# Optimization experiments

Hardware: AMD Instinct MI355X
Metric: run time of the kernel (lower is better)

Reference implementation:

```python
import jax, jax.numpy as jnp
import numpy as np


def _prelu(x, alpha):
    # PReLU with alpha shared over H,W (per-channel alpha, shape (C,))
    return jnp.where(x >= 0, x, alpha * x)


def _maxpool_2x2_s1_same(x):
    # TF MaxPooling2D(pool_size=2, strides=1, padding='same'): pad bottom/right
    return jax.lax.reduce_window(
        x, -jnp.inf, jax.lax.max,
        window_dimensions=(1, 2, 2, 1), window_strides=(1, 1, 1, 1),
        padding=[(0, 0), (0, 1), (0, 1), (0, 0)])


def _down_sample(x, W, b, alpha):
    # 1x1 Conv2D stride 2 'same' == subsample then channel matmul
    y = jnp.einsum('bhwc,cd->bhwd', x[:, ::2, ::2, :], W) + b
    y = _prelu(y, alpha)
    return _maxpool_2x2_s1_same(y)


def _up_sample(x, W, b, alpha):
    # 1x1 Conv2DTranspose stride 2 'same': even positions get conv output, rest only bias
    B, H, Wd, C = x.shape
    y = jnp.einsum('bhwc,cd->bhwd', x, W)
    z = jnp.zeros((B, 2 * H, 2 * Wd, C), dtype=x.dtype).at[:, ::2, ::2, :].set(y) + b
    z = _prelu(z, alpha)
    return _maxpool_2x2_s1_same(z)


def setup_inputs() -> dict:
    key = jax.random.key(0)
    ks = jax.random.split(key, 12)
    B, H, C = 8, 512, 3
    return {
        'input1': jax.random.normal(ks[0], (B, 2 * H, 2 * H, C), jnp.float32),
        'input2': jax.random.normal(ks[1], (B, H, H, C), jnp.float32),
        'input3': jax.random.normal(ks[2], (B, H // 2, H // 2, C), jnp.float32),
        'W_down': jax.random.normal(ks[3], (C, C), jnp.float32) * 0.5,
        'b_down': jax.random.normal(ks[4], (C,), jnp.float32) * 0.1,
        'alpha_down': jax.random.uniform(ks[5], (C,), jnp.float32) * 0.25,
        'W_up': jax.random.normal(ks[6], (C, C), jnp.float32) * 0.5,
        'b_up': jax.random.normal(ks[7], (C,), jnp.float32) * 0.1,
        'alpha_up': jax.random.uniform(ks[8], (C,), jnp.float32) * 0.25,
        'W_c': jax.random.normal(ks[9], (C, C), jnp.float32) * 0.5,
        'b_c': jax.random.normal(ks[10], (C,), jnp.float32) * 0.1,
        'alpha_g': jax.random.uniform(ks[11], (C,), jnp.float32) * 0.25,
        'scale': 2,
    }


def reference(input1, input2, input3, W_down, b_down, alpha_down,
              W_up, b_up, alpha_up, W_c, b_c, alpha_g, scale):
    assert scale == 2, 'only scale=2 path is well-defined in the source'
    i1 = _down_sample(input1, W_down, b_down, alpha_down)  # (B,H,W,C)
    i2 = input2
    i3 = _up_sample(input3, W_up, b_up, alpha_up)          # (B,H,W,C)

    s = i1 + i2 + i3
    g = jnp.mean(s, axis=(1, 2), keepdims=True)            # GlobalAvgPool, (B,1,1,C)

    conv1x1 = lambda t: jnp.einsum('bhwc,cd->bhwd', t, W_c) + b_c
    x = _prelu(conv1x1(g), alpha_g)
    # self.conv2d is the SAME layer applied three times -> c1 == c2 == c3,
    # hence y1 == y2 == y3; compute once (identical math).
    y = jax.nn.softmax(conv1x1(x), axis=-1)                # (B,1,1,C)
    return y * i1 + y * i2 + y * i3
```

## Files before the change

kernel.cpp:

```cpp
#include <hip/hip_runtime.h>

#define HW 512
#define NB 8

__device__ __forceinline__ float prelu(float x, float a) { return x >= 0.f ? x : a * x; }

__global__ __launch_bounds__(256) void k1_compute_s(
    const float* __restrict__ in1, const float* __restrict__ in2, const float* __restrict__ in3,
    const float* __restrict__ Wd, const float* __restrict__ bd, const float* __restrict__ ad,
    const float* __restrict__ Wu, const float* __restrict__ bu, const float* __restrict__ au,
    float* __restrict__ s_out, float* __restrict__ partials)
{
    const int b  = blockIdx.z;
    const int h0 = blockIdx.y * 16, w0 = blockIdx.x * 16;
    const int tid = threadIdx.x;

    __shared__ float d1[17][17][3];

    for (int idx = tid; idx < 17 * 17; idx += 256) {
        const int ty = idx / 17, tx = idx % 17;
        const int gh = h0 + ty, gw = w0 + tx;
        float v0 = -INFINITY, v1 = -INFINITY, v2 = -INFINITY;
        if (gh < HW && gw < HW) {
            const float* p = in1 + (((b * 1024 + 2 * gh) * 1024 + 2 * gw) * 3);
            const float x0 = p[0], x1 = p[1], x2 = p[2];
            v0 = prelu(x0 * Wd[0] + x1 * Wd[3] + x2 * Wd[6] + bd[0], ad[0]);
            v1 = prelu(x0 * Wd[1] + x1 * Wd[4] + x2 * Wd[7] + bd[1], ad[1]);
            v2 = prelu(x0 * Wd[2] + x1 * Wd[5] + x2 * Wd[8] + bd[2], ad[2]);
        }
        d1[ty][tx][0] = v0; d1[ty][tx][1] = v1; d1[ty][tx][2] = v2;
    }
    __syncthreads();

    const int ty = tid >> 4, tx = tid & 15;
    const int h = h0 + ty, w = w0 + tx;

    float i1c0 = fmaxf(fmaxf(d1[ty][tx][0], d1[ty][tx + 1][0]),
                       fmaxf(d1[ty + 1][tx][0], d1[ty + 1][tx + 1][0]));
    float i1c1 = fmaxf(fmaxf(d1[ty][tx][1], d1[ty][tx + 1][1]),
                       fmaxf(d1[ty + 1][tx][1], d1[ty + 1][tx + 1][1]));
    float i1c2 = fmaxf(fmaxf(d1[ty][tx][2], d1[ty][tx + 1][2]),
                       fmaxf(d1[ty + 1][tx][2], d1[ty + 1][tx + 1][2]));

    const float cu0 = prelu(bu[0], au[0]);
    const float cu1 = prelu(bu[1], au[1]);
    const float cu2 = prelu(bu[2], au[2]);
    float i3c0 = cu0, i3c1 = cu1, i3c2 = cu2;
    const int he = h + (h & 1), we = w + (w & 1);
    if (he < HW && we < HW) {
        const float* p = in3 + (((b * 256 + (he >> 1)) * 256 + (we >> 1)) * 3);
        const float x0 = p[0], x1 = p[1], x2 = p[2];
        i3c0 = fmaxf(i3c0, prelu(x0 * Wu[0] + x1 * Wu[3] + x2 * Wu[6] + bu[0], au[0]));
        i3c1 = fmaxf(i3c1, prelu(x0 * Wu[1] + x1 * Wu[4] + x2 * Wu[7] + bu[1], au[1]));
        i3c2 = fmaxf(i3c2, prelu(x0 * Wu[2] + x1 * Wu[5] + x2 * Wu[8] + bu[2], au[2]));
    }

    const int pix = ((b * HW + h) * HW + w) * 3;
    float s0 = i1c0 + in2[pix + 0] + i3c0;
    float s1 = i1c1 + in2[pix + 1] + i3c1;
    float s2 = i1c2 + in2[pix + 2] + i3c2;

    s_out[pix + 0] = s0; s_out[pix + 1] = s1; s_out[pix + 2] = s2;

    #pragma unroll
    for (int off = 32; off > 0; off >>= 1) {
        s0 += __shfl_down(s0, off);
        s1 += __shfl_down(s1, off);
        s2 += __shfl_down(s2, off);
    }
    __shared__ float red[4][3];
    const int lane = tid & 63, wave = tid >> 6;
    if (lane == 0) { red[wave][0] = s0; red[wave][1] = s1; red[wave][2] = s2; }
    __syncthreads();
    if (tid == 0) {
        const int pid = (b * 32 + blockIdx.y) * 32 + blockIdx.x;
        partials[pid * 3 + 0] = red[0][0] + red[1][0] + red[2][0] + red[3][0];
        partials[pid * 3 + 1] = red[0][1] + red[1][1] + red[2][1] + red[3][1];
        partials[pid * 3 + 2] = red[0][2] + red[1][2] + red[2][2] + red[3][2];
    }
}

__global__ __launch_bounds__(256) void k2_gate(
    const float* __restrict__ partials,
    const float* __restrict__ Wc, const float* __restrict__ bc, const float* __restrict__ ag,
    float* __restrict__ y)
{
    const int b = blockIdx.x;
    const int tid = threadIdx.x;
    float s0 = 0.f, s1 = 0.f, s2 = 0.f;
    for (int i = tid; i < 1024; i += 256) {
        const float* p = partials + (b * 1024 + i) * 3;
        s0 += p[0]; s1 += p[1]; s2 += p[2];
    }
    #pragma unroll
    for (int off = 32; off > 0; off >>= 1) {
        s0 += __shfl_down(s0, off);
        s1 += __shfl_down(s1, off);
        s2 += __shfl_down(s2, off);
    }
    __shared__ float red[4][3];
    const int lane = tid & 63, wave = tid >> 6;
    if (lane == 0) { red[wave][0] = s0; red[wave][1] = s1; red[wave][2] = s2; }
    __syncthreads();
    if (tid == 0) {
        const float inv_n = 1.f / (float)(HW * HW);
        const float g0 = (red[0][0] + red[1][0] + red[2][0] + red[3][0]) * inv_n;
        const float g1 = (red[0][1] + red[1][1] + red[2][1] + red[3][1]) * inv_n;
        const float g2 = (red[0][2] + red[1][2] + red[2][2] + red[3][2]) * inv_n;
        const float x0 = prelu(g0 * Wc[0] + g1 * Wc[3] + g2 * Wc[6] + bc[0], ag[0]);
        const float x1 = prelu(g0 * Wc[1] + g1 * Wc[4] + g2 * Wc[7] + bc[1], ag[1]);
        const float x2 = prelu(g0 * Wc[2] + g1 * Wc[5] + g2 * Wc[8] + bc[2], ag[2]);
        const float q0 = x0 * Wc[0] + x1 * Wc[3] + x2 * Wc[6] + bc[0];
        const float q1 = x0 * Wc[1] + x1 * Wc[4] + x2 * Wc[7] + bc[1];
        const float q2 = x0 * Wc[2] + x1 * Wc[5] + x2 * Wc[8] + bc[2];
        const float m = fmaxf(q0, fmaxf(q1, q2));
        const float e0 = expf(q0 - m), e1 = expf(q1 - m), e2 = expf(q2 - m);
        const float inv = 1.f / (e0 + e1 + e2);
        y[b * 3 + 0] = e0 * inv;
        y[b * 3 + 1] = e1 * inv;
        y[b * 3 + 2] = e2 * inv;
    }
}

__global__ __launch_bounds__(256) void k3_scale(float* __restrict__ out, const float* __restrict__ y)
{
    const int i = blockIdx.x * 256 + threadIdx.x;
    const int f = i * 4;
    const int b = f / (HW * HW * 3);
    const int c0 = f % 3;
    const float* yb = y + b * 3;
    const float m0 = yb[c0];
    const float m1 = yb[c0 == 2 ? 0 : c0 + 1];
    const float m2 = yb[c0 == 0 ? 2 : c0 - 1];
    float4 v = reinterpret_cast<float4*>(out)[i];
    v.x *= m0; v.y *= m1; v.z *= m2; v.w *= m0;
    reinterpret_cast<float4*>(out)[i] = v;
}

extern "C" void kernel_launch(void* const* d_in, const int* in_sizes, int n_in,
                              void* d_out, int out_size, void* d_ws, size_t ws_size,
                              hipStream_t stream)
{
    const float* in1 = (const float*)d_in[0];
    const float* in2 = (const float*)d_in[1];
    const float* in3 = (const float*)d_in[2];
    const float* Wd  = (const float*)d_in[3];
    const float* bd  = (const float*)d_in[4];
    const float* ad  = (const float*)d_in[5];
    const float* Wu  = (const float*)d_in[6];
    const float* bu  = (const float*)d_in[7];
    const float* au  = (const float*)d_in[8];
    const float* Wc  = (const float*)d_in[9];
    const float* bc  = (const float*)d_in[10];
    const float* ag  = (const float*)d_in[11];
    float* out = (float*)d_out;

    float* partials = (float*)d_ws;
    float* y        = partials + 8192 * 3;

    k1_compute_s<<<dim3(32, 32, NB), 256, 0, stream>>>(in1, in2, in3, Wd, bd, ad, Wu, bu, au, out, partials);
    k2_gate<<<NB, 256, 0, stream>>>(partials, Wc, bc, ag, y);
    k3_scale<<<6144, 256, 0, stream>>>(out, y);
}
```

Baseline: 39.07 us.

## Fuse all stages into one cooperative kernel holding the sum in LDS

Replaces the three-kernel pipeline with a single cooperative-launch kernel of 256 blocks of 1024 threads. Each block handles a 16-row stripe of one batch image, keeps the intermediate sum in shared memory, and performs a grid-wide sync before computing the gate and writing scaled output directly. This removes the global write and re-read of the intermediate sum plus two extra launches, at the cost of a grid barrier, about 117KB of LDS per block and one block per CU. The old kernels remain as a fallback if the cooperative launch fails.

New measurement: 84.42 us. +116.1%, slower.

```diff
diff --git a/kernel.cpp b/kernel.cpp
--- a/kernel.cpp
+++ b/kernel.cpp
@@ -1,9 +1,143 @@
 #include <hip/hip_runtime.h>
+#include <hip/hip_cooperative_groups.h>
+
+namespace cg = cooperative_groups;
 
 #define HW 512
-#define NB 8
 
 __device__ __forceinline__ float prelu(float x, float a) { return x >= 0.f ? x : a * x; }
+
+__global__ __launch_bounds__(1024) void fused(
+    const float* __restrict__ in1, const float* __restrict__ in2, const float* __restrict__ in3,
+    const float* __restrict__ Wd, const float* __restrict__ bd, const float* __restrict__ ad,
+    const float* __restrict__ Wu, const float* __restrict__ bu, const float* __restrict__ au,
+    const float* __restrict__ Wc, const float* __restrict__ bc, const float* __restrict__ ag,
+    float* __restrict__ out, float* __restrict__ ws)
+{
+    extern __shared__ float smem[];
+    float* s_lds = smem;
+    float* d1    = smem + 24576;
+    float* red   = d1 + 4617;
+    float* ybuf  = red + 48;
+
+    const int tid    = threadIdx.x;
+    const int bid    = blockIdx.x;
+    const int batch  = bid >> 5;
+    const int stripe = bid & 31;
+    const int r0     = stripe * 16;
+
+    float wd[9], wu[9];
+    #pragma unroll
+    for (int k = 0; k < 9; k++) { wd[k] = Wd[k]; wu[k] = Wu[k]; }
+    const float bd0 = bd[0], bd1 = bd[1], bd2 = bd[2];
+    const float ad0 = ad[0], ad1 = ad[1], ad2 = ad[2];
+    const float bu0 = bu[0], bu1 = bu[1], bu2 = bu[2];
+    const float au0 = au[0], au1 = au[1], au2 = au[2];
+    const float cu0 = prelu(bu0, au0), cu1 = prelu(bu1, au1), cu2 = prelu(bu2, au2);
+
+    float p0 = 0.f, p1 = 0.f, p2 = 0.f;
+    const int lrOff = tid >> 9;
+    const int col   = tid & 511;
+
+    for (int i = 0; i < 8; i++) {
+        const int drStart = (i == 0) ? 0 : (2 * i + 1);
+        const int n = (2 * i + 2 - drStart + 1) * 513;
+        __syncthreads();
+        for (int e = tid; e < n; e += 1024) {
+            const int dr = drStart + e / 513;
+            const int c  = e - (e / 513) * 513;
+            const int gh = r0 + dr;
+            float v0 = -INFINITY, v1 = -INFINITY, v2 = -INFINITY;
+            if (gh < HW && c < HW) {
+                const float* p = in1 + ((batch * 1024 + 2 * gh) * 1024 + 2 * c) * 3;
+                const float x0 = p[0], x1 = p[1], x2 = p[2];
+                v0 = prelu(x0 * wd[0] + x1 * wd[3] + x2 * wd[6] + bd0, ad0);
+                v1 = prelu(x0 * wd[1] + x1 * wd[4] + x2 * wd[7] + bd1, ad1);
+                v2 = prelu(x0 * wd[2] + x1 * wd[5] + x2 * wd[8] + bd2, ad2);
+            }
+            float* q = d1 + (dr % 3) * 1539 + c * 3;
+            q[0] = v0; q[1] = v1; q[2] = v2;
+        }
+        __syncthreads();
+
+        const int lr  = 2 * i + lrOff;
+        const int row = r0 + lr;
+        const float* ra = d1 + (lr % 3) * 1539 + col * 3;
+        const float* rb = d1 + ((lr + 1) % 3) * 1539 + col * 3;
+        float i1c0 = fmaxf(fmaxf(ra[0], ra[3]), fmaxf(rb[0], rb[3]));
+        float i1c1 = fmaxf(fmaxf(ra[1], ra[4]), fmaxf(rb[1], rb[4]));
+        float i1c2 = fmaxf(fmaxf(ra[2], ra[5]), fmaxf(rb[2], rb[5]));
+
+        float i3c0 = cu0, i3c1 = cu1, i3c2 = cu2;
+        const int he = row + (row & 1), we = col + (col & 1);
+        if (he < HW && we < HW) {
+            const float* p = in3 + ((batch * 256 + (he >> 1)) * 256 + (we >> 1)) * 3;
+            const float x0 = p[0], x1 = p[1], x2 = p[2];
+            i3c0 = fmaxf(i3c0, prelu(x0 * wu[0] + x1 * wu[3] + x2 * wu[6] + bu0, au0));
+            i3c1 = fmaxf(i3c1, prelu(x0 * wu[1] + x1 * wu[4] + x2 * wu[7] + bu1, au1));
+            i3c2 = fmaxf(i3c2, prelu(x0 * wu[2] + x1 * wu[5] + x2 * wu[8] + bu2, au2));
+        }
+
+        const float* q2 = in2 + ((batch * HW + row) * HW + col) * 3;
+        const float s0 = i1c0 + q2[0] + i3c0;
+        const float s1 = i1c1 + q2[1] + i3c1;
+        const float s2 = i1c2 + q2[2] + i3c2;
+        float* qs = s_lds + (lr * 512 + col) * 3;
+        qs[0] = s0; qs[1] = s1; qs[2] = s2;
+        p0 += s0; p1 += s1; p2 += s2;
+    }
+
+    #pragma unroll
+    for (int off = 32; off > 0; off >>= 1) {
+        p0 += __shfl_down(p0, off);
+        p1 += __shfl_down(p1, off);
+        p2 += __shfl_down(p2, off);
+    }
+    const int lane = tid & 63, wv = tid >> 6;
+    if (lane == 0) { red[wv * 3 + 0] = p0; red[wv * 3 + 1] = p1; red[wv * 3 + 2] = p2; }
+    __syncthreads();
+    if (tid == 0) {
+        float t0 = 0.f, t1 = 0.f, t2 = 0.f;
+        for (int k = 0; k < 16; k++) { t0 += red[k * 3]; t1 += red[k * 3 + 1]; t2 += red[k * 3 + 2]; }
+        ws[bid * 3 + 0] = t0; ws[bid * 3 + 1] = t1; ws[bid * 3 + 2] = t2;
+        __threadfence();
+    }
+
+    cg::this_grid().sync();
+
+    if (tid == 0) {
+        float g0 = 0.f, g1 = 0.f, g2 = 0.f;
+        const float* pw = ws + batch * 96;
+        for (int k = 0; k < 32; k++) { g0 += pw[k * 3]; g1 += pw[k * 3 + 1]; g2 += pw[k * 3 + 2]; }
+        const float inv_n = 1.f / (float)(HW * HW);
+        g0 *= inv_n; g1 *= inv_n; g2 *= inv_n;
+        const float x0 = prelu(g0 * Wc[0] + g1 * Wc[3] + g2 * Wc[6] + bc[0], ag[0]);
+        const float x1 = prelu(g0 * Wc[1] + g1 * Wc[4] + g2 * Wc[7] + bc[1], ag[1]);
+        const float x2 = prelu(g0 * Wc[2] + g1 * Wc[5] + g2 * Wc[8] + bc[2], ag[2]);
+        const float q0 = x0 * Wc[0] + x1 * Wc[3] + x2 * Wc[6] + bc[0];
+        const float q1 = x0 * Wc[1] + x1 * Wc[4] + x2 * Wc[7] + bc[1];
+        const float q2 = x0 * Wc[2] + x1 * Wc[5] + x2 * Wc[8] + bc[2];
+        const float m  = fmaxf(q0, fmaxf(q1, q2));
+        const float e0 = expf(q0 - m), e1 = expf(q1 - m), e2 = expf(q2 - m);
+        const float inv = 1.f / (e0 + e1 + e2);
+        ybuf[0] = e0 * inv; ybuf[1] = e1 * inv; ybuf[2] = e2 * inv;
+    }
+    __syncthreads();
+    const float ym[3] = { ybuf[0], ybuf[1], ybuf[2] };
+
+    float4* og = (float4*)(out + (size_t)bid * 24576);
+    #pragma unroll
+    for (int k = 0; k < 6; k++) {
+        const int idx = k * 1024 + tid;
+        const int c0  = idx % 3;
+        float4 v = *((const float4*)s_lds + idx);
+        v.x *= ym[c0];
+        v.y *= ym[c0 == 2 ? 0 : c0 + 1];
+        v.z *= ym[c0 == 0 ? 2 : c0 - 1];
+        v.w *= ym[c0];
+        og[idx] = v;
+    }
+}
 
 __global__ __launch_bounds__(256) void k1_compute_s(
     const float* __restrict__ in1, const float* __restrict__ in2, const float* __restrict__ in3,
@@ -14,9 +148,7 @@
     const int b  = blockIdx.z;
     const int h0 = blockIdx.y * 16, w0 = blockIdx.x * 16;
     const int tid = threadIdx.x;
-
     __shared__ float d1[17][17][3];
-
     for (int idx = tid; idx < 17 * 17; idx += 256) {
         const int ty = idx / 17, tx = idx % 17;
         const int gh = h0 + ty, gw = w0 + tx;
@@ -31,20 +163,12 @@
         d1[ty][tx][0] = v0; d1[ty][tx][1] = v1; d1[ty][tx][2] = v2;
     }
     __syncthreads();
-
     const int ty = tid >> 4, tx = tid & 15;
     const int h = h0 + ty, w = w0 + tx;
-
-    float i1c0 = fmaxf(fmaxf(d1[ty][tx][0], d1[ty][tx + 1][0]),
-                       fmaxf(d1[ty + 1][tx][0], d1[ty + 1][tx + 1][0]));
-    float i1c1 = fmaxf(fmaxf(d1[ty][tx][1], d1[ty][tx + 1][1]),
-                       fmaxf(d1[ty + 1][tx][1], d1[ty + 1][tx + 1][1]));
-    float i1c2 = fmaxf(fmaxf(d1[ty][tx][2], d1[ty][tx + 1][2]),
-                       fmaxf(d1[ty + 1][tx][2], d1[ty + 1][tx + 1][2]));
-
-    const float cu0 = prelu(bu[0], au[0]);
-    const float cu1 = prelu(bu[1], au[1]);
-    const float cu2 = prelu(bu[2], au[2]);
+    float i1c0 = fmaxf(fmaxf(d1[ty][tx][0], d1[ty][tx + 1][0]), fmaxf(d1[ty + 1][tx][0], d1[ty + 1][tx + 1][0]));
+    float i1c1 = fmaxf(fmaxf(d1[ty][tx][1], d1[ty][tx + 1][1]), fmaxf(d1[ty + 1][tx][1], d1[ty + 1][tx + 1][1]));
+    float i1c2 = fmaxf(fmaxf(d1[ty][tx][2], d1[ty][tx + 1][2]), fmaxf(d1[ty + 1][tx][2], d1[ty + 1][tx + 1][2]));
+    const float cu0 = prelu(bu[0], au[0]), cu1 = prelu(bu[1], au[1]), cu2 = prelu(bu[2], au[2]);
     float i3c0 = cu0, i3c1 = cu1, i3c2 = cu2;
     const int he = h + (h & 1), we = w + (w & 1);
     if (he < HW && we < HW) {
@@ -54,19 +178,14 @@
         i3c1 = fmaxf(i3c1, prelu(x0 * Wu[1] + x1 * Wu[4] + x2 * Wu[7] + bu[1], au[1]));
         i3c2 = fmaxf(i3c2, prelu(x0 * Wu[2] + x1 * Wu[5] + x2 * Wu[8] + bu[2], au[2]));
     }
-
     const int pix = ((b * HW + h) * HW + w) * 3;
     float s0 = i1c0 + in2[pix + 0] + i3c0;
     float s1 = i1c1 + in2[pix + 1] + i3c1;
     float s2 = i1c2 + in2[pix + 2] + i3c2;
-
     s_out[pix + 0] = s0; s_out[pix + 1] = s1; s_out[pix + 2] = s2;
-
     #pragma unroll
     for (int off = 32; off > 0; off >>= 1) {
-        s0 += __shfl_down(s0, off);
-        s1 += __shfl_down(s1, off);
-        s2 += __shfl_down(s2, off);
+        s0 += __shfl_down(s0, off); s1 += __shfl_down(s1, off); s2 += __shfl_down(s2, off);
     }
     __shared__ float red[4][3];
     const int lane = tid & 63, wave = tid >> 6;
@@ -94,9 +213,7 @@
     }
     #pragma unroll
     for (int off = 32; off > 0; off >>= 1) {
-        s0 += __shfl_down(s0, off);
-        s1 += __shfl_down(s1, off);
-        s2 += __shfl_down(s2, off);
+        s0 += __shfl_down(s0, off); s1 += __shfl_down(s1, off); s2 += __shfl_down(s2, off);
     }
     __shared__ float red[4][3];
     const int lane = tid & 63, wave = tid >> 6;
@@ -116,9 +233,7 @@
         const float m = fmaxf(q0, fmaxf(q1, q2));
         const float e0 = expf(q0 - m), e1 = expf(q1 - m), e2 = expf(q2 - m);
         const float inv = 1.f / (e0 + e1 + e2);
-        y[b * 3 + 0] = e0 * inv;
-        y[b * 3 + 1] = e1 * inv;
-        y[b * 3 + 2] = e2 * inv;
+        y[b * 3 + 0] = e0 * inv; y[b * 3 + 1] = e1 * inv; y[b * 3 + 2] = e2 * inv;
     }
 }
 
@@ -154,11 +269,21 @@
     const float* bc  = (const float*)d_in[10];
     const float* ag  = (const float*)d_in[11];
     float* out = (float*)d_out;
-
-    float* partials = (float*)d_ws;
-    float* y        = partials + 8192 * 3;
-
-    k1_compute_s<<<dim3(32, 32, NB), 256, 0, stream>>>(in1, in2, in3, Wd, bd, ad, Wu, bu, au, out, partials);
-    k2_gate<<<NB, 256, 0, stream>>>(partials, Wc, bc, ag, y);
-    k3_scale<<<6144, 256, 0, stream>>>(out, y);
-}
+    float* ws  = (float*)d_ws;
+
+    void* args[] = { (void*)&in1, (void*)&in2, (void*)&in3,
+                     (void*)&Wd, (void*)&bd, (void*)&ad,
+                     (void*)&Wu, (void*)&bu, (void*)&au,
+                     (void*)&Wc, (void*)&bc, (void*)&ag,
+                     (void*)&out, (void*)&ws };
+    const unsigned smem_bytes = (24576 + 4617 + 48 + 3 + 4) * sizeof(float);
+    hipError_t err = hipLaunchCooperativeKernel((const void*)fused, dim3(256), dim3(1024),
+                                                args, smem_bytes, stream);
+    if (err != hipSuccess) {
+        float* partials = ws;
+        float* y        = partials + 8192 * 3;
+        k1_compute_s<<<dim3(32, 32, 8), 256, 0, stream>>>(in1, in2, in3, Wd, bd, ad, Wu, bu, au, out, partials);
+        k2_gate<<<8, 256, 0, stream>>>(partials, Wc, bc, ag, y);
+        k3_scale<<<6144, 256, 0, stream>>>(out, y);
+    }
+}
```

## Widen k1 tiles to 4 pixels per thread and fuse gate into scale kernel

Applied to the files above, without the earlier changes.

The first kernel now has each thread handle 4 consecutive pixels in a 16x64 tile. Weights are held in registers, and the in2 reads and s writes use float4 vector accesses, so there are fewer partial sums. The gate computation is folded into the scaling kernel: every block recomputes the per-batch softmax from 256 partials. This removes one launch and the separate y buffer. The cost is redundant gate math in each of 1024 blocks, plus more register use and a higher LDS footprint per block.

Measured after the change: 42.67 us. 9.2% more time.

```diff
diff --git a/kernel.cpp b/kernel.cpp
--- a/kernel.cpp
+++ b/kernel.cpp
@@ -1,7 +1,7 @@
 #include <hip/hip_runtime.h>
 
 #define HW 512
-#define NB 8
+#define D1_PITCH 197
 
 __device__ __forceinline__ float prelu(float x, float a) { return x >= 0.f ? x : a * x; }
 
@@ -11,130 +11,175 @@
     const float* __restrict__ Wu, const float* __restrict__ bu, const float* __restrict__ au,
     float* __restrict__ s_out, float* __restrict__ partials)
 {
-    const int b  = blockIdx.z;
-    const int h0 = blockIdx.y * 16, w0 = blockIdx.x * 16;
-    const int tid = threadIdx.x;
-
-    __shared__ float d1[17][17][3];
-
-    for (int idx = tid; idx < 17 * 17; idx += 256) {
-        const int ty = idx / 17, tx = idx % 17;
-        const int gh = h0 + ty, gw = w0 + tx;
-        float v0 = -INFINITY, v1 = -INFINITY, v2 = -INFINITY;
-        if (gh < HW && gw < HW) {
-            const float* p = in1 + (((b * 1024 + 2 * gh) * 1024 + 2 * gw) * 3);
+    __shared__ float d1[17 * D1_PITCH];
+    __shared__ float red[4][3];
+
+    const int tid   = threadIdx.x;
+    const int bx    = blockIdx.x;
+    const int by    = blockIdx.y;
+    const int batch = blockIdx.z;
+    const int h0    = by * 16;
+    const int w0b   = bx * 64;
+
+    float wd[9], wu[9];
+    #pragma unroll
+    for (int k = 0; k < 9; k++) { wd[k] = Wd[k]; wu[k] = Wu[k]; }
+    const float bd0 = bd[0], bd1 = bd[1], bd2 = bd[2];
+    const float ad0 = ad[0], ad1 = ad[1], ad2 = ad[2];
+    const float bu0 = bu[0], bu1 = bu[1], bu2 = bu[2];
+    const float au0 = au[0], au1 = au[1], au2 = au[2];
+    const float cu0 = prelu(bu0, au0), cu1 = prelu(bu1, au1), cu2 = prelu(bu2, au2);
+
+    #pragma unroll
+    for (int k = 0; k < 5; ++k) {
+        const int e = k * 256 + tid;
+        if (e < 17 * 65) {
+            const int dr = e / 65, dc = e - dr * 65;
+            const int gh = h0 + dr, gw = w0b + dc;
+            float v0 = -INFINITY, v1 = -INFINITY, v2 = -INFINITY;
+            if (gh < HW && gw < HW) {
+                const float* p = in1 + ((size_t)((batch * 1024 + 2 * gh) * 1024 + 2 * gw)) * 3;
+                const float x0 = p[0], x1 = p[1], x2 = p[2];
+                v0 = prelu(x0 * wd[0] + x1 * wd[3] + x2 * wd[6] + bd0, ad0);
+                v1 = prelu(x0 * wd[1] + x1 * wd[4] + x2 * wd[7] + bd1, ad1);
+                v2 = prelu(x0 * wd[2] + x1 * wd[5] + x2 * wd[8] + bd2, ad2);
+            }
+            float* q = d1 + dr * D1_PITCH + dc * 3;
+            q[0] = v0; q[1] = v1; q[2] = v2;
+        }
+    }
+    __syncthreads();
+
+    const int r  = tid >> 4;
+    const int cg = tid & 15;
+    const int h  = h0 + r;
+    const int w0 = w0b + cg * 4;
+
+    const float* in2p = in2 + ((size_t)((batch * HW + h) * HW + w0)) * 3;
+    float i2v[12];
+    #pragma unroll
+    for (int k = 0; k < 3; ++k)
+        *reinterpret_cast<float4*>(&i2v[4 * k]) = reinterpret_cast<const float4*>(in2p)[k];
+
+    const int he = h + (h & 1);
+    const bool heok = he < HW;
+    const int w3 = w0 >> 1;
+    float ud[3][3];
+    #pragma unroll
+    for (int k = 0; k < 3; ++k) {
+        float u0 = cu0, u1 = cu1, u2 = cu2;
+        if (heok && (w3 + k) < 256) {
+            const float* p = in3 + ((size_t)((batch * 256 + (he >> 1)) * 256 + w3 + k)) * 3;
             const float x0 = p[0], x1 = p[1], x2 = p[2];
-            v0 = prelu(x0 * Wd[0] + x1 * Wd[3] + x2 * Wd[6] + bd[0], ad[0]);
-            v1 = prelu(x0 * Wd[1] + x1 * Wd[4] + x2 * Wd[7] + bd[1], ad[1]);
-            v2 = prelu(x0 * Wd[2] + x1 * Wd[5] + x2 * Wd[8] + bd[2], ad[2]);
-        }
-        d1[ty][tx][0] = v0; d1[ty][tx][1] = v1; d1[ty][tx][2] = v2;
-    }
-    __syncthreads();
-
-    const int ty = tid >> 4, tx = tid & 15;
-    const int h = h0 + ty, w = w0 + tx;
-
-    float i1c0 = fmaxf(fmaxf(d1[ty][tx][0], d1[ty][tx + 1][0]),
-                       fmaxf(d1[ty + 1][tx][0], d1[ty + 1][tx + 1][0]));
-    float i1c1 = fmaxf(fmaxf(d1[ty][tx][1], d1[ty][tx + 1][1]),
-                       fmaxf(d1[ty + 1][tx][1], d1[ty + 1][tx + 1][1]));
-    float i1c2 = fmaxf(fmaxf(d1[ty][tx][2], d1[ty][tx + 1][2]),
-                       fmaxf(d1[ty + 1][tx][2], d1[ty + 1][tx + 1][2]));
-
-    const float cu0 = prelu(bu[0], au[0]);
-    const float cu1 = prelu(bu[1], au[1]);
-    const float cu2 = prelu(bu[2], au[2]);
-    float i3c0 = cu0, i3c1 = cu1, i3c2 = cu2;
-    const int he = h + (h & 1), we = w + (w & 1);
-    if (he < HW && we < HW) {
-        const float* p = in3 + (((b * 256 + (he >> 1)) * 256 + (we >> 1)) * 3);
-        const float x0 = p[0], x1 = p[1], x2 = p[2];
-        i3c0 = fmaxf(i3c0, prelu(x0 * Wu[0] + x1 * Wu[3] + x2 * Wu[6] + bu[0], au[0]));
-        i3c1 = fmaxf(i3c1, prelu(x0 * Wu[1] + x1 * Wu[4] + x2 * Wu[7] + bu[1], au[1]));
-        i3c2 = fmaxf(i3c2, prelu(x0 * Wu[2] + x1 * Wu[5] + x2 * Wu[8] + bu[2], au[2]));
-    }
-
-    const int pix = ((b * HW + h) * HW + w) * 3;
-    float s0 = i1c0 + in2[pix + 0] + i3c0;
-    float s1 = i1c1 + in2[pix + 1] + i3c1;
-    float s2 = i1c2 + in2[pix + 2] + i3c2;
-
-    s_out[pix + 0] = s0; s_out[pix + 1] = s1; s_out[pix + 2] = s2;
+            u0 = fmaxf(u0, prelu(x0 * wu[0] + x1 * wu[3] + x2 * wu[6] + bu0, au0));
+            u1 = fmaxf(u1, prelu(x0 * wu[1] + x1 * wu[4] + x2 * wu[7] + bu1, au1));
+            u2 = fmaxf(u2, prelu(x0 * wu[2] + x1 * wu[5] + x2 * wu[8] + bu2, au2));
+        }
+        ud[k][0] = u0; ud[k][1] = u1; ud[k][2] = u2;
+    }
+
+    const int baseA = r * D1_PITCH + cg * 12;
+    const int baseB = baseA + D1_PITCH;
+    float pA0 = d1[baseA + 0], pA1 = d1[baseA + 1], pA2 = d1[baseA + 2];
+    float pB0 = d1[baseB + 0], pB1 = d1[baseB + 1], pB2 = d1[baseB + 2];
+
+    float s[4][3];
+    float sum0 = 0.f, sum1 = 0.f, sum2 = 0.f;
+    #pragma unroll
+    for (int j = 0; j < 4; ++j) {
+        const int o = 3 * (j + 1);
+        const float cA0 = d1[baseA + o], cA1 = d1[baseA + o + 1], cA2 = d1[baseA + o + 2];
+        const float cB0 = d1[baseB + o], cB1 = d1[baseB + o + 1], cB2 = d1[baseB + o + 2];
+        const int uk = (j + 1) >> 1;
+        const float s0 = fmaxf(fmaxf(pA0, cA0), fmaxf(pB0, cB0)) + i2v[3 * j + 0] + ud[uk][0];
+        const float s1 = fmaxf(fmaxf(pA1, cA1), fmaxf(pB1, cB1)) + i2v[3 * j + 1] + ud[uk][1];
+        const float s2 = fmaxf(fmaxf(pA2, cA2), fmaxf(pB2, cB2)) + i2v[3 * j + 2] + ud[uk][2];
+        s[j][0] = s0; s[j][1] = s1; s[j][2] = s2;
+        sum0 += s0; sum1 += s1; sum2 += s2;
+        pA0 = cA0; pA1 = cA1; pA2 = cA2;
+        pB0 = cB0; pB1 = cB1; pB2 = cB2;
+    }
+
+    float* outp = s_out + ((size_t)((batch * HW + h) * HW + w0)) * 3;
+    #pragma unroll
+    for (int k = 0; k < 3; ++k) {
+        float4 v;
+        v.x = s[(4 * k + 0) / 3][(4 * k + 0) % 3];
+        v.y = s[(4 * k + 1) / 3][(4 * k + 1) % 3];
+        v.z = s[(4 * k + 2) / 3][(4 * k + 2) % 3];
+        v.w = s[(4 * k + 3) / 3][(4 * k + 3) % 3];
+        reinterpret_cast<float4*>(outp)[k] = v;
+    }
 
     #pragma unroll
     for (int off = 32; off > 0; off >>= 1) {
-        s0 += __shfl_down(s0, off);
-        s1 += __shfl_down(s1, off);
-        s2 += __shfl_down(s2, off);
-    }
-    __shared__ float red[4][3];
-    const int lane = tid & 63, wave = tid >> 6;
-    if (lane == 0) { red[wave][0] = s0; red[wave][1] = s1; red[wave][2] = s2; }
+        sum0 += __shfl_down(sum0, off);
+        sum1 += __shfl_down(sum1, off);
+        sum2 += __shfl_down(sum2, off);
+    }
+    if ((tid & 63) == 0) { red[tid >> 6][0] = sum0; red[tid >> 6][1] = sum1; red[tid >> 6][2] = sum2; }
     __syncthreads();
     if (tid == 0) {
-        const int pid = (b * 32 + blockIdx.y) * 32 + blockIdx.x;
+        const int pid = (batch * 32 + by) * 8 + bx;
         partials[pid * 3 + 0] = red[0][0] + red[1][0] + red[2][0] + red[3][0];
         partials[pid * 3 + 1] = red[0][1] + red[1][1] + red[2][1] + red[3][1];
         partials[pid * 3 + 2] = red[0][2] + red[1][2] + red[2][2] + red[3][2];
     }
 }
 
-__global__ __launch_bounds__(256) void k2_gate(
+__global__ __launch_bounds__(256) void k2_gate_scale(
     const float* __restrict__ partials,
     const float* __restrict__ Wc, const float* __restrict__ bc, const float* __restrict__ ag,
-    float* __restrict__ y)
+    float* __restrict__ out)
 {
-    const int b = blockIdx.x;
-    const int tid = threadIdx.x;
-    float s0 = 0.f, s1 = 0.f, s2 = 0.f;
-    for (int i = tid; i < 1024; i += 256) {
-        const float* p = partials + (b * 1024 + i) * 3;
-        s0 += p[0]; s1 += p[1]; s2 += p[2];
-    }
-    #pragma unroll
-    for (int off = 32; off > 0; off >>= 1) {
-        s0 += __shfl_down(s0, off);
-        s1 += __shfl_down(s1, off);
-        s2 += __shfl_down(s2, off);
-    }
-    __shared__ float red[4][3];
-    const int lane = tid & 63, wave = tid >> 6;
-    if (lane == 0) { red[wave][0] = s0; red[wave][1] = s1; red[wave][2] = s2; }
+    __shared__ float ybuf[3];
+    const int bid   = blockIdx.x;
+    const int batch = bid >> 7;
+    const int chunk = bid & 127;
+    const int tid   = threadIdx.x;
+
+    if (tid < 64) {
+        const float* pw = partials + batch * 256 * 3;
+        float g0 = 0.f, g1 = 0.f, g2 = 0.f;
+        #pragma unroll
+        for (int k = 0; k < 4; ++k) {
+            const float* p = pw + (tid + 64 * k) * 3;
+            g0 += p[0]; g1 += p[1]; g2 += p[2];
+        }
+        #pragma unroll
+        for (int off = 32; off > 0; off >>= 1) {
+            g0 += __shfl_down(g0, off);
+            g1 += __shfl_down(g1, off);
+            g2 += __shfl_down(g2, off);
+        }
+        if (tid == 0) {
+            const float inv_n = 1.f / (float)(HW * HW);
+            g0 *= inv_n; g1 *= inv_n; g2 *= inv_n;
+            const float x0 = prelu(g0 * Wc[0] + g1 * Wc[3] + g2 * Wc[6] + bc[0], ag[0]);
+            const float x1 = prelu(g0 * Wc[1] + g1 * Wc[4] + g2 * Wc[7] + bc[1], ag[1]);
+            const float x2 = prelu(g0 * Wc[2] + g1 * Wc[5] + g2 * Wc[8] + bc[2], ag[2]);
+            const float q0 = x0 * Wc[0] + x1 * Wc[3] + x2 * Wc[6] + bc[0];
+            const float q1 = x0 * Wc[1] + x1 * Wc[4] + x2 * Wc[7] + bc[1];
+            const float q2 = x0 * Wc[2] + x1 * Wc[5] + x2 * Wc[8] + bc[2];
+            const float m  = fmaxf(q0, fmaxf(q1, q2));
+            const float e0 = expf(q0 - m), e1 = expf(q1 - m), e2 = expf(q2 - m);
+            const float inv = 1.f / (e0 + e1 + e2);
+            ybuf[0] = e0 * inv; ybuf[1] = e1 * inv; ybuf[2] = e2 * inv;
+        }
+    }
     __syncthreads();
-    if (tid == 0) {
-        const float inv_n = 1.f / (float)(HW * HW);
-        const float g0 = (red[0][0] + red[1][0] + red[2][0] + red[3][0]) * inv_n;
-        const float g1 = (red[0][1] + red[1][1] + red[2][1] + red[3][1]) * inv_n;
-        const float g2 = (red[0][2] + red[1][2] + red[2][2] + red[3][2]) * inv_n;
-        const float x0 = prelu(g0 * Wc[0] + g1 * Wc[3] + g2 * Wc[6] + bc[0], ag[0]);
-        const float x1 = prelu(g0 * Wc[1] + g1 * Wc[4] + g2 * Wc[7] + bc[1], ag[1]);
-        const float x2 = prelu(g0 * Wc[2] + g1 * Wc[5] + g2 * Wc[8] + bc[2], ag[2]);
-        const float q0 = x0 * Wc[0] + x1 * Wc[3] + x2 * Wc[6] + bc[0];
-        const float q1 = x0 * Wc[1] + x1 * Wc[4] + x2 * Wc[7] + bc[1];
-        const float q2 = x0 * Wc[2] + x1 * Wc[5] + x2 * Wc[8] + bc[2];
-        const float m = fmaxf(q0, fmaxf(q1, q2));
-        const float e0 = expf(q0 - m), e1 = expf(q1 - m), e2 = expf(q2 - m);
-        const float inv = 1.f / (e0 + e1 + e2);
-        y[b * 3 + 0] = e0 * inv;
-        y[b * 3 + 1] = e1 * inv;
-        y[b * 3 + 2] = e2 * inv;
-    }
-}
-
-__global__ __launch_bounds__(256) void k3_scale(float* __restrict__ out, const float* __restrict__ y)
-{
-    const int i = blockIdx.x * 256 + threadIdx.x;
-    const int f = i * 4;
-    const int b = f / (HW * HW * 3);
-    const int c0 = f % 3;
-    const float* yb = y + b * 3;
-    const float m0 = yb[c0];
-    const float m1 = yb[c0 == 2 ? 0 : c0 + 1];
-    const float m2 = yb[c0 == 0 ? 2 : c0 - 1];
-    float4 v = reinterpret_cast<float4*>(out)[i];
-    v.x *= m0; v.y *= m1; v.z *= m2; v.w *= m0;
-    reinterpret_cast<float4*>(out)[i] = v;
+    const float ym[3] = { ybuf[0], ybuf[1], ybuf[2] };
+
+    float* p = out + ((size_t)batch * 262144 + chunk * 2048 + tid * 8) * 3;
+    #pragma unroll
+    for (int k = 0; k < 6; ++k) {
+        float4 v = reinterpret_cast<float4*>(p)[k];
+        v.x *= ym[(4 * k + 0) % 3];
+        v.y *= ym[(4 * k + 1) % 3];
+        v.z *= ym[(4 * k + 2) % 3];
+        v.w *= ym[(4 * k + 3) % 3];
+        reinterpret_cast<float4*>(p)[k] = v;
+    }
 }
 
 extern "C" void kernel_launch(void* const* d_in, const int* in_sizes, int n_in,
@@ -154,11 +199,8 @@
     const float* bc  = (const float*)d_in[10];
     const float* ag  = (const float*)d_in[11];
     float* out = (float*)d_out;
-
     float* partials = (float*)d_ws;
-    float* y        = partials + 8192 * 3;
-
-    k1_compute_s<<<dim3(32, 32, NB), 256, 0, stream>>>(in1, in2, in3, Wd, bd, ad, Wu, bu, au, out, partials);
-    k2_gate<<<NB, 256, 0, stream>>>(partials, Wc, bc, ag, y);
-    k3_scale<<<6144, 256, 0, stream>>>(out, y);
+
+    k1_compute_s<<<dim3(8, 32, 8), 256, 0, stream>>>(in1, in2, in3, Wd, bd, ad, Wu, bu, au, out, partials);
+    k2_gate_scale<<<1024, 256, 0, stream>>>(partials, Wc, bc, ag, out);
 }
```
